# Kernel tuning notes

Hardware: AMD Instinct MI355X
Metric: run time of the kernel (lower is better)

## Reference

```python
import jax, jax.numpy as jnp
import numpy as np

S, B, N, A, L = 2, 8, 12, 4, 24
C, AUX, EK, K, M, OTH = 256, 16, 64, 256, 8, 32
D2 = C + AUX          # transfromer2 d_model
FF = 2048             # torch TransformerEncoderLayer default dim_feedforward
RIN = 2 * EK + 2 * D2 + 2 * OTH
NLAYERS = 2


def _layernorm(x, g, b, eps=1e-5):
    mu = x.mean(-1, keepdims=True)
    var = ((x - mu) ** 2).mean(-1, keepdims=True)
    return (x - mu) * jax.lax.rsqrt(var + eps) * g + b


def _mha(x, Wq, bq, Wk, bk, Wv, bv, Wo, bo):
    # x: [seq, batch, d]; single head (nhead=1), torch seq-first semantics
    q = x @ Wq.T + bq
    k = x @ Wk.T + bk
    v = x @ Wv.T + bv
    scale = x.shape[-1] ** -0.5
    att = jax.nn.softmax(jnp.einsum('sbd,tbd->bst', q, k) * scale, axis=-1)
    o = jnp.einsum('bst,tbd->sbd', att, v)
    return o @ Wo.T + bo


def _encoder(x, aw, ab, w1, b1, w2, b2, lg, lb):
    # post-norm torch TransformerEncoderLayer, ReLU FFN, dropout off (eval)
    for i in range(aw.shape[0]):
        a = _mha(x, aw[i, 0], ab[i, 0], aw[i, 1], ab[i, 1], aw[i, 2], ab[i, 2], aw[i, 3], ab[i, 3])
        x = _layernorm(x + a, lg[i, 0], lb[i, 0])
        h = jax.nn.relu(x @ w1[i].T + b1[i]) @ w2[i].T + b2[i]
        x = _layernorm(x + h, lg[i, 1], lb[i, 1])
    return x


def _conv(x, w, b, pad):
    y = jax.lax.conv_general_dilated(x, w, (1, 1), [(pad, pad), (0, 0)],
                                     dimension_numbers=('NCHW', 'OIHW', 'NCHW'))
    return y + b[None, :, None, None]


def _forward(chars, att_type, kw_idx, input_idx, static, other,
             char_table, filter_w, filter_b, gate_w, gate_b, mlp_w, mlp_b,
             kw_table, aline_w, aline_b,
             t1_attn_w, t1_attn_b, t1_ffn_w1, t1_ffn_b1, t1_ffn_w2, t1_ffn_b2, t1_ln_g, t1_ln_b,
             t2_attn_w, t2_attn_b, t2_ffn_w1, t2_ffn_b1, t2_ffn_w2, t2_ffn_b2, t2_ln_g, t2_ln_b,
             reg_w1, reg_b1, reg_w2, reg_b2):
    # nn.Embedding(max_norm=1): rows renormalized to norm <= 1
    nrm = jnp.linalg.norm(char_table, axis=1, keepdims=True)
    tbl = char_table * jnp.minimum(1.0, 1.0 / jnp.maximum(nrm, 1e-7))
    ce = tbl[chars]                                  # [S,B,N,A,L,C]
    x = ce.reshape(-1, 1, L, C)                      # strings as conv batch
    f = jnp.tanh(_conv(x, filter_w, filter_b, 1))    # gated conv: tanh * sigmoid
    g = jax.nn.sigmoid(_conv(x, gate_w, gate_b, 1))
    v = _conv(f * g, mlp_w, mlp_b, 0)                # 1x1 conv back to 1 channel
    str_vec = v.reshape(S, B, N, A, L, C).mean(axis=4)   # mean over chars -> [S,B,N,A,C]
    kw_vec = kw_table[kw_idx] @ aline_w.T + aline_b      # keyword path -> [S,B,N,A,C]
    att_vec = jnp.where((att_type == 1)[..., None], kw_vec, str_vec)
    # transfromer1: torch seq-first, seq = nodes, batch = (side, plan, attr)
    x1 = att_vec.transpose(2, 0, 1, 3, 4).reshape(N, S * B * A, C)
    y1 = _encoder(x1, t1_attn_w, t1_attn_b, t1_ffn_w1, t1_ffn_b1, t1_ffn_w2, t1_ffn_b2, t1_ln_g, t1_ln_b)
    node_enc = y1.reshape(N, S, B, A, C).mean(axis=3).transpose(1, 2, 0, 3)  # mean over attrs -> [S,B,N,C]
    h = jnp.concatenate([node_enc, static], axis=-1)                          # [S,B,N,D2]
    # transfromer2: seq = plan batch, batch = (side, node) -- torch seq-first
    x2 = h.transpose(1, 0, 2, 3).reshape(B, S * N, D2)
    y2 = _encoder(x2, t2_attn_w, t2_attn_b, t2_ffn_w1, t2_ffn_b1, t2_ffn_w2, t2_ffn_b2, t2_ln_g, t2_ln_b)
    real = y2.reshape(B, S, N, D2).mean(axis=2)      # mean over nodes -> [B,S,D2]
    inp = kw_table[input_idx].mean(axis=2)           # encoding_input -> [S,B,EK]
    feats = jnp.concatenate([inp[0], real[:, 0], inp[1], real[:, 1], other], axis=1)  # [B,RIN]
    return jax.nn.relu(feats @ reg_w1.T + reg_b1) @ reg_w2.T + reg_b2  # [B,1]


def setup_inputs() -> dict:
    key = jax.random.key(0)
    ks = iter(jax.random.split(key, 64))
    def rn(shape, s=0.02):
        return jax.random.normal(next(ks), shape, jnp.float32) * s
    inp = {
        'chars': jax.random.randint(next(ks), (S, B, N, A, L), 0, 128, jnp.int32),
        'att_type': jax.random.randint(next(ks), (S, B, N, A), 0, 2, jnp.int32),
        'kw_idx': jax.random.randint(next(ks), (S, B, N, A), 0, K, jnp.int32),
        'input_idx': jax.random.randint(next(ks), (S, B, M), 0, K, jnp.int32),
        'static': rn((S, B, N, AUX), 1.0),
        'other': rn((B, 2 * OTH), 1.0),
        'char_table': rn((128, C), 1.0),
        'filter_w': rn((16, 1, 3, 1), 0.2), 'filter_b': rn((16,), 0.02),
        'gate_w': rn((16, 1, 3, 1), 0.2), 'gate_b': rn((16,), 0.02),
        'mlp_w': rn((1, 16, 1, 1), 0.2), 'mlp_b': rn((1,), 0.02),
        'kw_table': rn((K, EK), 0.05),
        'aline_w': rn((C, EK), 0.05), 'aline_b': rn((C,), 0.02),
        't1_attn_w': rn((NLAYERS, 4, C, C), 0.05), 't1_attn_b': rn((NLAYERS, 4, C), 0.02),
        't1_ffn_w1': rn((NLAYERS, FF, C), 0.02), 't1_ffn_b1': rn((NLAYERS, FF), 0.02),
        't1_ffn_w2': rn((NLAYERS, C, FF), 0.02), 't1_ffn_b2': rn((NLAYERS, C), 0.02),
        't1_ln_g': jnp.ones((NLAYERS, 2, C), jnp.float32), 't1_ln_b': jnp.zeros((NLAYERS, 2, C), jnp.float32),
        't2_attn_w': rn((NLAYERS, 4, D2, D2), 0.05), 't2_attn_b': rn((NLAYERS, 4, D2), 0.02),
        't2_ffn_w1': rn((NLAYERS, FF, D2), 0.02), 't2_ffn_b1': rn((NLAYERS, FF), 0.02),
        't2_ffn_w2': rn((NLAYERS, D2, FF), 0.02), 't2_ffn_b2': rn((NLAYERS, D2), 0.02),
        't2_ln_g': jnp.ones((NLAYERS, 2, D2), jnp.float32), 't2_ln_b': jnp.zeros((NLAYERS, 2, D2), jnp.float32),
        'reg_w1': rn((32, RIN), 0.05), 'reg_b1': rn((32,), 0.02),
        'reg_w2': rn((1, 32), 0.1), 'reg_b2': rn((1,), 0.02),
    }
    return inp


def reference(chars, att_type, kw_idx, input_idx, static, other,
              char_table, filter_w, filter_b, gate_w, gate_b, mlp_w, mlp_b,
              kw_table, aline_w, aline_b,
              t1_attn_w, t1_attn_b, t1_ffn_w1, t1_ffn_b1, t1_ffn_w2, t1_ffn_b2, t1_ln_g, t1_ln_b,
              t2_attn_w, t2_attn_b, t2_ffn_w1, t2_ffn_b1, t2_ffn_w2, t2_ffn_b2, t2_ln_g, t2_ln_b,
              reg_w1, reg_b1, reg_w2, reg_b2):
    return _forward(chars, att_type, kw_idx, input_idx, static, other,
                    char_table, filter_w, filter_b, gate_w, gate_b, mlp_w, mlp_b,
                    kw_table, aline_w, aline_b,
                    t1_attn_w, t1_attn_b, t1_ffn_w1, t1_ffn_b1, t1_ffn_w2, t1_ffn_b2, t1_ln_g, t1_ln_b,
                    t2_attn_w, t2_attn_b, t2_ffn_w1, t2_ffn_b1, t2_ffn_w2, t2_ffn_b2, t2_ln_g, t2_ln_b,
                    reg_w1, reg_b1, reg_w2, reg_b2)
```

## Files before the change

### kernel.cpp

```cpp
#include <hip/hip_runtime.h>
#include <math.h>

#define S_ 2
#define B_ 8
#define N_ 12
#define A_ 4
#define L_ 24
#define C_ 256
#define AUX_ 16
#define EK_ 64
#define K_ 256
#define M_ 8
#define OTH_ 32
#define D2_ 272
#define FF_ 2048
#define RIN_ 736
#define NSTR_ (S_*B_*N_*A_)
#define NCVT_ 256
#define T4_ (5441536/4)
#define CSZ_ (T4_/NCVT_)

typedef __attribute__((ext_vector_type(8))) short short8v;
typedef __attribute__((ext_vector_type(4))) float f32x4;

// ... 57 lines not shown
        if (tid == 0) su = atomicAdd(ctr, 1);
        __syncthreads();
        int item = su;
        if (item >= NSTR_ + NCVT_) break;

        if (item >= NSTR_) {
            int base = (item - NSTR_) * CSZ_;
            #pragma unroll
            for (int i = 0; i < 6; ++i) {
                int q = base + i * 1024 + tid;
                if (q < base + CSZ_) {
                    int idx = q * 4;
                    const float* src; int off;
                    if      (idx < 524288)  { src = s0; off = 0; }
                    else if (idx < 1572864) { src = s1; off = 524288; }
                    else if (idx < 2621440) { src = s2; off = 1572864; }
                    else if (idx < 3213312) { src = s3; off = 2621440; }
                    else if (idx < 4327424) { src = s4; off = 3213312; }
                    else                    { src = s5; off = 4327424; }
                    float4 v = *(const float4*)(src + (idx - off));
                    ushort4 o;
                    o.x = f2bf(v.x); o.y = f2bf(v.y); o.z = f2bf(v.z); o.w = f2bf(v.w);
                    *(ushort4*)(wdst + idx) = o;
                }
            }
            continue;
        }

        int str = item;
        bool kw = (att_type[str] == 1);
        float partial;
        if (kw) {
            const float* kr = kwt + kw_idx[str] * EK_ + grp * 16;
            const float* awr = aw + c * EK_ + grp * 16;
            float acc = (grp == 0) ? ab[c] : 0.f;
            #pragma unroll
            for (int e = 0; e < 16; ++e) acc = fmaf(kr[e], awr[e], acc);
            partial = acc;
        } else {
            if (tid < L_) ch[tid] = chars[str * L_ + tid];
            __syncthreads();
            #pragma unroll
            for (int i = 0; i < 6; ++i) {
                int l = grp * 6 + i;
                xv[l + 1][c] = tblS[ch[l] * C_ + c];
            }
            if (grp == 0) xv[0][c] = 0.f;
            if (grp == 3) xv[L_ + 1][c] = 0.f;
            __syncthreads();

            float osum[4] = {0.f, 0.f, 0.f, 0.f};
            float xm = xv[0][c], x0 = xv[1][c];
            for (int l = 1; l <= L_; ++l) {
                float xp = xv[l + 1][c];
                #pragma unroll
                for (int oo = 0; oo < 4; ++oo) {
                    float pf2 = fbv[oo] + f0[oo]*xm + f1[oo]*x0 + f2[oo]*xp;
                    float pg  = gbv[oo] + g0[oo]*xm + g1[oo]*x0 + g2[oo]*xp;
                    pf2 = fminf(fmaxf(pf2, -43.f), 43.f);
                    pg  = fminf(fmaxf(pg,  -22.f), 22.f);
                    float e1 = __builtin_amdgcn_exp2f(pf2);
                    float e2 = __builtin_amdgcn_exp2f(pg);
                    float num = (e1 - 1.f) * e2;
                    float den = (e1 + 1.f) * (e2 + 1.f);
                    osum[oo] = fmaf(num, __builtin_amdgcn_rcpf(den), osum[oo]);
                }
                xm = x0; x0 = xp;
            }
            partial = mwv[0]*osum[0] + mwv[1]*osum[1] + mwv[2]*osum[2] + mwv[3]*osum[3];
        }
        part[grp][c] = partial;
        __syncthreads();
        if (grp == 0) {
            int a = str & 3;
            int n = (str >> 2) % N_;
            int sb = str / (N_ * A_);
            int row = n * 64 + sb * 4 + a;
            float tot = part[0][c] + part[1][c] + part[2][c] + part[3][c];
            float out = kw ? tot : (mb[0] + tot * (1.f / 24.f));
            x1[row * C_ + c] = out;
            x1b[row * C_ + c] = f2bf(out);
        }
    }
}

__global__ void gemm_mfma_k(const unsigned short* __restrict__ Ab,
                            const unsigned short* __restrict__ Wb,
                            const float* __restrict__ bias,
                            float* __restrict__ Cf, unsigned short* __restrict__ Cb,
                            int R, int K, int N, int relu, int kslice, int obf) {
    int tid = threadIdx.x;
    int wave = tid >> 6, lane = tid & 63;
    int fr = lane & 15, fq = lane >> 4;
    int m0 = blockIdx.y * 64;
    int n0 = blockIdx.x * 64 + wave * 16;
    int kbeg = blockIdx.z * kslice;
    int kend = min(kbeg + kslice, K);
    int col = n0 + fr;
    bool bok = col < N;
    const unsigned short* Wrow = Wb + (size_t)col * K;
    const unsigned short* Ar0 = Ab + (size_t)(m0 + fr) * K;
    const unsigned short* Ar1 = Ab + (size_t)(m0 + 16 + fr) * K;
    const unsigned short* Ar2 = Ab + (size_t)(m0 + 32 + fr) * K;
    const unsigned short* Ar3 = Ab + (size_t)(m0 + 48 + fr) * K;

    f32x4 acc0 = {0.f,0.f,0.f,0.f}, acc1 = {0.f,0.f,0.f,0.f};
    f32x4 acc2 = {0.f,0.f,0.f,0.f}, acc3 = {0.f,0.f,0.f,0.f};
    const short8v z8 = {0,0,0,0,0,0,0,0};
    short8v pb0, pa00, pa01, pa02, pa03;
    short8v pb1, pa10, pa11, pa12, pa13;

#define LDSET(PB,PA0,PA1,PA2,PA3,ktv) do {                                \
        int kl2 = (ktv) + fq * 8;                                         \
        bool kv2 = (kl2 + 8 <= kend);                                     \
        PB  = (bok && kv2) ? *(const short8v*)(Wrow + kl2) : z8;          \
        PA0 = kv2 ? *(const short8v*)(Ar0 + kl2) : z8;                    \
        PA1 = kv2 ? *(const short8v*)(Ar1 + kl2) : z8;                    \
        PA2 = kv2 ? *(const short8v*)(Ar2 + kl2) : z8;                    \
        PA3 = kv2 ? *(const short8v*)(Ar3 + kl2) : z8;                    \
    } while (0)

    if (kbeg < kend) {
        LDSET(pb0, pa00, pa01, pa02, pa03, kbeg);
        LDSET(pb1, pa10, pa11, pa12, pa13, kbeg + 32);
        for (int kt = kbeg; kt < kend; kt += 64) {
            short8v tb = pb0, t0 = pa00, t1 = pa01, t2 = pa02, t3 = pa03;
            LDSET(pb0, pa00, pa01, pa02, pa03, kt + 64);
            acc0 = __builtin_amdgcn_mfma_f32_16x16x32_bf16(t0, tb, acc0, 0, 0, 0);
            acc1 = __builtin_amdgcn_mfma_f32_16x16x32_bf16(t1, tb, acc1, 0, 0, 0);
            acc2 = __builtin_amdgcn_mfma_f32_16x16x32_bf16(t2, tb, acc2, 0, 0, 0);
            acc3 = __builtin_amdgcn_mfma_f32_16x16x32_bf16(t3, tb, acc3, 0, 0, 0);
            short8v ub = pb1, u0 = pa10, u1 = pa11, u2 = pa12, u3 = pa13;
            LDSET(pb1, pa10, pa11, pa12, pa13, kt + 96);
            acc0 = __builtin_amdgcn_mfma_f32_16x16x32_bf16(u0, ub, acc0, 0, 0, 0);
            acc1 = __builtin_amdgcn_mfma_f32_16x16x32_bf16(u1, ub, acc1, 0, 0, 0);
            acc2 = __builtin_amdgcn_mfma_f32_16x16x32_bf16(u2, ub, acc2, 0, 0, 0);
            acc3 = __builtin_amdgcn_mfma_f32_16x16x32_bf16(u3, ub, acc3, 0, 0, 0);
        }
    }
#undef LDSET

    if (!bok) return;
    bool direct = (gridDim.z == 1);
    float bv = direct ? bias[col] : 0.f;
    float* outf = direct ? Cf : (Cf + (size_t)blockIdx.z * R * N);
#define STOREACC(accv, mi) do {                                           \
        _Pragma("unroll")                                                 \
        for (int j = 0; j < 4; ++j) {                                     \
            int row = m0 + (mi)*16 + fq * 4 + j;                          \
            float v = accv[j] + bv;                                       \
            if (direct && relu) v = fmaxf(v, 0.f);                        \
            if (direct && obf) Cb[(size_t)row * N + col] = f2bf(v);       \
            else               outf[(size_t)row * N + col] = v;           \
        }                                                                 \
    } while (0)
    STOREACC(acc0, 0); STOREACC(acc1, 1); STOREACC(acc2, 2); STOREACC(acc3, 3);
#undef STOREACC
}

__global__ void redln_k(const float* __restrict__ part, const float* __restrict__ bias,
                        float* __restrict__ x, unsigned short* __restrict__ xb,
                        const float* __restrict__ g, const float* __restrict__ b,
                        int d, int NS, int RN) {
    int r = blockIdx.x, tid = threadIdx.x;
    __shared__ float red[10];
    const float* xr = x + (size_t)r * d;
    int i0 = tid, i1 = tid + 256;
    bool h0 = i0 < d, h1 = i1 < d;
    float v0 = 0.f, v1 = 0.f;
    if (h0) {
        v0 = xr[i0] + bias[i0];
        for (int z = 0; z < NS; ++z) v0 += part[(size_t)z * RN + (size_t)r * d + i0];
    }
    if (h1) {
        v1 = xr[i1] + bias[i1];
        for (int z = 0; z < NS; ++z) v1 += part[(size_t)z * RN + (size_t)r * d + i1];
    }
    float s = v0 + v1, ss = v0 * v0 + v1 * v1;
    for (int off = 32; off; off >>= 1) {
        s += __shfl_down(s, off);
        ss += __shfl_down(ss, off);
    }
    if ((tid & 63) == 0) { red[(tid >> 6) * 2] = s; red[(tid >> 6) * 2 + 1] = ss; }
    __syncthreads();
    if (tid == 0) {
        float S = red[0] + red[2] + red[4] + red[6];
        float SS = red[1] + red[3] + red[5] + red[7];
        float mu = S / d;
        float var = SS / d - mu * mu;
        red[8] = mu;
        red[9] = rsqrtf(var + 1e-5f);
    }
    __syncthreads();
    float mu = red[8], inv = red[9];
    float* xw = x + (size_t)r * d;
    if (h0) {
        float o = (v0 - mu) * inv * g[i0] + b[i0];
        xw[i0] = o; xb[(size_t)r * d + i0] = f2bf(o);
    }
    if (h1) {
        float o = (v1 - mu) * inv * g[i1] + b[i1];
        xw[i1] = o; xb[(size_t)r * d + i1] = f2bf(o);
    }
}

__global__ void attn_k(const float* __restrict__ qkv, unsigned short* __restrict__ ob,
                       int seq, int batch, int d, float scale) {
    __shared__ float sm[3 * 12 * 260];
    __shared__ float sc[12 * 12];
    int j = blockIdx.x, tid = threadIdx.x;
    int dp = d + 4;
    int s3 = 3 * d;
    float* qs = sm;
    float* ks = sm + 12 * 260;
    float* vs = sm + 2 * 12 * 260;
    for (int idx = tid; idx < seq * d; idx += 256) {
        int s = idx / d, cc = idx - s * d;
        const float* base = qkv + (size_t)(s * batch + j) * s3 + cc;
        qs[s * dp + cc] = base[0];
        ks[s * dp + cc] = base[d];
        vs[s * dp + cc] = base[2 * d];
    }
    __syncthreads();
    for (int p4 = tid; p4 < seq * seq * 4; p4 += 256) {
        int p = p4 >> 2, sub = p4 & 3;
        int s = p / seq, t = p - s * seq;
        const float* qp = qs + s * dp;
        const float* kp = ks + t * dp;
        float acc = 0.f;
        for (int cc = sub; cc < d; cc += 4) acc = fmaf(qp[cc], kp[cc], acc);
        acc += __shfl_xor(acc, 1);
        acc += __shfl_xor(acc, 2);
        if (sub == 0) sc[p] = acc * scale;
    }
    __syncthreads();
    if (tid < seq) {
        float m = -1e30f;
        for (int t = 0; t < seq; ++t) m = fmaxf(m, sc[tid * seq + t]);
        float ssum = 0.f;
        for (int t = 0; t < seq; ++t) {
            float e = __expf(sc[tid * seq + t] - m);
            sc[tid * seq + t] = e;
            ssum += e;
        }
        float inv = 1.f / ssum;
        for (int t = 0; t < seq; ++t) sc[tid * seq + t] *= inv;
    }
    __syncthreads();
    for (int c = tid; c < d; c += 256) {
        for (int s = 0; s < seq; ++s) {
            float acc = 0.f;
            for (int t = 0; t < seq; ++t) acc = fmaf(sc[s * seq + t], vs[t * dp + c], acc);
            ob[(size_t)(s * batch + j) * d + c] = f2bf(acc);
        }
    }
}

__global__ void build_x2_k(const float* __restrict__ y1, const float* __restrict__ stat,
                           float* __restrict__ x2, unsigned short* __restrict__ x2b) {
    int id = blockIdx.x;
    int n = id % N_;
    int b = (id / N_) % B_;
    int s = id / (N_ * B_);
    int orow = b * (S_ * N_) + s * N_ + n;
    for (int c = threadIdx.x; c < D2_; c += 256) {
        float v;
        if (c < C_) {
            int j0 = (s * B_ + b) * A_;
            float acc = 0.f;
            for (int a = 0; a < A_; ++a) acc += y1[(size_t)(n * 64 + j0 + a) * C_ + c];
            v = acc * 0.25f;
        } else {
            v = stat[((size_t)(s * B_ + b) * N_ + n) * AUX_ + (c - C_)];
        }
        x2[(size_t)orow * D2_ + c] = v;
        x2b[(size_t)orow * D2_ + c] = f2bf(v);
    }
}

__global__ void regressor_k(const float* __restrict__ y2, const int* __restrict__ input_idx,
                            const float* __restrict__ kwt, const float* __restrict__ other,
                            const float* __restrict__ w1, const float* __restrict__ b1,
                            const float* __restrict__ w2, const float* __restrict__ b2,
                            float* __restrict__ out) {
    int b = blockIdx.x;
    int tid = threadIdx.x;
    __shared__ float realsh[2][D2_];
    __shared__ float feats[RIN_];
    __shared__ float hh[32];
    for (int idx = tid; idx < 2 * D2_; idx += 256) {
        int s = idx / D2_, c = idx - s * D2_;
        float acc = 0.f;
        for (int n = 0; n < N_; ++n)
            acc += y2[(size_t)(b * 24 + s * N_ + n) * D2_ + c];
        realsh[s][c] = acc * (1.f / 12.f);
    }
    __syncthreads();
    for (int i = tid; i < RIN_; i += 256) {
        float v;
        if (i < 64) {
            float acc = 0.f;
            for (int m = 0; m < M_; ++m) acc += kwt[input_idx[b * M_ + m] * EK_ + i];
            v = acc * 0.125f;
        } else if (i < 336) {
            v = realsh[0][i - 64];
        } else if (i < 400) {
            int e = i - 336;
            float acc = 0.f;
            for (int m = 0; m < M_; ++m) acc += kwt[input_idx[64 + b * M_ + m] * EK_ + e];
            v = acc * 0.125f;
        } else if (i < 672) {
            v = realsh[1][i - 400];
        } else {
            v = other[b * 64 + (i - 672)];
        }
        feats[i] = v;
    }
    __syncthreads();
    if (tid < 32) {
        float acc = b1[tid];
        const float* wr = w1 + (size_t)tid * RIN_;
        for (int i = 0; i < RIN_; ++i) acc += feats[i] * wr[i];
        hh[tid] = fmaxf(acc, 0.f);
    }
    __syncthreads();
    if (tid == 0) {
        float acc = b2[0];
        for (int j = 0; j < 32; ++j) acc += hh[j] * w2[j];
        out[b] = acc;
    }
}

extern "C" void kernel_launch(void* const* d_in, const int* in_sizes, int n_in,
                              void* d_out, int out_size, void* d_ws, size_t ws_size,
                              hipStream_t stream) {
    const int*   chars      = (const int*)d_in[0];
    const int*   att_type   = (const int*)d_in[1];
    const int*   kw_idx     = (const int*)d_in[2];
    const int*   input_idx  = (const int*)d_in[3];
    const float* stat       = (const float*)d_in[4];
    const float* other      = (const float*)d_in[5];
    const float* char_table = (const float*)d_in[6];
    const float* filter_w   = (const float*)d_in[7];
    const float* filter_b   = (const float*)d_in[8];
    const float* gate_w     = (const float*)d_in[9];
    const float* gate_b     = (const float*)d_in[10];
    const float* mlp_w      = (const float*)d_in[11];
    const float* mlp_b      = (const float*)d_in[12];
    const float* kw_table   = (const float*)d_in[13];
    const float* aline_w    = (const float*)d_in[14];
    const float* aline_b    = (const float*)d_in[15];
    const float* t1_attn_w  = (const float*)d_in[16];
    const float* t1_attn_b  = (const float*)d_in[17];
    const float* t1_ffn_w1  = (const float*)d_in[18];
    const float* t1_ffn_b1  = (const float*)d_in[19];
    const float* t1_ffn_w2  = (const float*)d_in[20];
    const float* t1_ffn_b2  = (const float*)d_in[21];
    const float* t1_ln_g    = (const float*)d_in[22];
    const float* t1_ln_b    = (const float*)d_in[23];
    const float* t2_attn_w  = (const float*)d_in[24];
    const float* t2_attn_b  = (const float*)d_in[25];
    const float* t2_ffn_w1  = (const float*)d_in[26];
    const float* t2_ffn_b1  = (const float*)d_in[27];
    const float* t2_ffn_w2  = (const float*)d_in[28];
    const float* t2_ffn_b2  = (const float*)d_in[29];
    const float* t2_ln_g    = (const float*)d_in[30];
    const float* t2_ln_b    = (const float*)d_in[31];
    const float* reg_w1     = (const float*)d_in[32];
    const float* reg_b1     = (const float*)d_in[33];
    const float* reg_w2     = (const float*)d_in[34];
    const float* reg_b2     = (const float*)d_in[35];

    float* ws   = (float*)d_ws;
    float* tblS = ws;
    float* x1   = tblS + 32768;
    float* qkv  = x1 + 196608;
    float* pbuf = qkv + 589824;
    float* x2   = pbuf + 786432;
    float* spare= x2 + 52224;
    unsigned short* x1b = (unsigned short*)(spare + 4352);
    unsigned short* obb = x1b + 196608;
    unsigned short* hb  = obb + 196608;
    unsigned short* x2b = hb + 1572864;
    unsigned short* wbf = x2b + 52224 + 16;
    unsigned short* wb_t1_attn = wbf;
    unsigned short* wb_t1_ffn1 = wbf + 524288;
    unsigned short* wb_t1_ffn2 = wbf + 1572864;
    unsigned short* wb_t2_attn = wbf + 2621440;
    unsigned short* wb_t2_ffn1 = wbf + 3213312;
    unsigned short* wb_t2_ffn2 = wbf + 4327424;
    int* ctr = (int*)(wbf + 5441536);

    auto gemm_f32 = [&](const unsigned short* A, const unsigned short* Wb, const float* bias,
                        float* Cc, int R, int Kk, int N) {
        dim3 g((N + 63) / 64, R / 64, 1);
        gemm_mfma_k<<<g, 256, 0, stream>>>(A, Wb, bias, Cc, (unsigned short*)0,
                                           R, Kk, N, 0, Kk, 0);
    };
    auto gemm_bf16 = [&](const unsigned short* A, const unsigned short* Wb, const float* bias,
                         unsigned short* Cc, int R, int Kk, int N) {
        dim3 g((N + 63) / 64, R / 64, 1);
        gemm_mfma_k<<<g, 256, 0, stream>>>(A, Wb, bias, (float*)0, Cc,
                                           R, Kk, N, 1, Kk, 1);
    };
    auto gemm_split_ln = [&](const unsigned short* A, const unsigned short* Wb,
                             const float* bias, float* x, unsigned short* xb,
                             const float* g, const float* b,
                             int R, int Kk, int N, int ns) {
        int ksl = ((Kk + ns - 1) / ns + 31) / 32 * 32;
        dim3 gr((N + 63) / 64, R / 64, ns);
        gemm_mfma_k<<<gr, 256, 0, stream>>>(A, Wb, bias, pbuf, (unsigned short*)0,
                                            R, Kk, N, 0, ksl, 0);
        redln_k<<<R, 256, 0, stream>>>(pbuf, bias, x, xb, g, b, N, ns, R * N);
    };

    hipMemsetAsync(ctr, 0, sizeof(int), stream);
    scale_table_k<<<128, 256, 0, stream>>>(char_table, tblS);
    attvec_k<<<512, 1024, 0, stream>>>(chars, att_type, kw_idx, tblS,
                                       filter_w, filter_b, gate_w, gate_b,
                                       mlp_w, mlp_b, kw_table, aline_w, aline_b,
                                       x1, x1b, ctr,
                                       t1_attn_w, t1_ffn_w1, t1_ffn_w2,
                                       t2_attn_w, t2_ffn_w1, t2_ffn_w2, wbf);

    for (int i = 0; i < 2; ++i) {
        const unsigned short* awb = wb_t1_attn + (size_t)i * 4 * C_ * C_;
        const float* ab = t1_attn_b + (size_t)i * 4 * C_;
        gemm_f32(x1b, awb, ab, qkv, 768, C_, 3 * C_);
        attn_k<<<64, 256, 0, stream>>>(qkv, obb, 12, 64, C_, 0.0625f);
        gemm_split_ln(obb, awb + 3 * C_ * C_, ab + 3 * C_, x1, x1b,
                      t1_ln_g + i * 2 * C_, t1_ln_b + i * 2 * C_, 768, C_, C_, 2);
        gemm_bf16(x1b, wb_t1_ffn1 + (size_t)i * FF_ * C_, t1_ffn_b1 + i * FF_, hb, 768, C_, FF_);
        gemm_split_ln(hb, wb_t1_ffn2 + (size_t)i * C_ * FF_, t1_ffn_b2 + i * C_, x1, x1b,
                      t1_ln_g + i * 2 * C_ + C_, t1_ln_b + i * 2 * C_ + C_, 768, FF_, C_, 4);
    }

    build_x2_k<<<192, 256, 0, stream>>>(x1, stat, x2, x2b);

    float sc2 = 1.0f / sqrtf(272.0f);
    for (int i = 0; i < 2; ++i) {
        const unsigned short* awb = wb_t2_attn + (size_t)i * 4 * D2_ * D2_;
        const float* ab = t2_attn_b + (size_t)i * 4 * D2_;
        gemm_f32(x2b, awb, ab, qkv, 192, D2_, 3 * D2_);
        attn_k<<<24, 256, 0, stream>>>(qkv, obb, 8, 24, D2_, sc2);
        gemm_split_ln(obb, awb + 3 * D2_ * D2_, ab + 3 * D2_, x2, x2b,
                      t2_ln_g + i * 2 * D2_, t2_ln_b + i * 2 * D2_, 192, D2_, D2_, 4);
        gemm_bf16(x2b, wb_t2_ffn1 + (size_t)i * FF_ * D2_, t2_ffn_b1 + i * FF_, hb, 192, D2_, FF_);
        gemm_split_ln(hb, wb_t2_ffn2 + (size_t)i * D2_ * FF_, t2_ffn_b2 + i * D2_, x2, x2b,
                      t2_ln_g + i * 2 * D2_ + D2_, t2_ln_b + i * 2 * D2_ + D2_, 192, FF_, D2_, 8);
    }

    regressor_k<<<8, 256, 0, stream>>>(x2, input_idx, kw_table, other,
                                       reg_w1, reg_b1, reg_w2, reg_b2, (float*)d_out);
}
```

Baseline: 321.8 us.

## Fuse QKV projection, attention, output projection and residual LayerNorm into one kernel

Replaces the four-launch attention sublayer (QKV GEMM, attention kernel, split-K output GEMM, and reduction plus LayerNorm) with one templated kernel per batch column. Each block computes its sequence's QKV with MFMA into shared memory, runs softmax attention, applies the output projection with MFMA, and does the residual add and LayerNorm in place. The aim is to cut launch overhead and the global round-trips of the qkv, attention output and partial-sum buffers. In exchange, each block reloads the full attention weights from L2, and only 64 or 24 blocks do the projection work, so GPU parallelism is lower.

```diff
diff --git a/kernel.cpp b/kernel.cpp
--- a/kernel.cpp
+++ b/kernel.cpp
@@ -285,54 +285,159 @@
     }
 }
 
-__global__ void attn_k(const float* __restrict__ qkv, unsigned short* __restrict__ ob,
-                       int seq, int batch, int d, float scale) {
-    __shared__ float sm[3 * 12 * 260];
-    __shared__ float sc[12 * 12];
-    int j = blockIdx.x, tid = threadIdx.x;
-    int dp = d + 4;
-    int s3 = 3 * d;
-    float* qs = sm;
-    float* ks = sm + 12 * 260;
-    float* vs = sm + 2 * 12 * 260;
-    for (int idx = tid; idx < seq * d; idx += 256) {
-        int s = idx / d, cc = idx - s * d;
-        const float* base = qkv + (size_t)(s * batch + j) * s3 + cc;
-        qs[s * dp + cc] = base[0];
-        ks[s * dp + cc] = base[d];
-        vs[s * dp + cc] = base[2 * d];
-    }
-    __syncthreads();
-    for (int p4 = tid; p4 < seq * seq * 4; p4 += 256) {
+template<int SEQ, int BATCH, int D>
+__global__ void attn_fused_k(const unsigned short* __restrict__ xb,
+                             float* __restrict__ x,
+                             const unsigned short* __restrict__ wqkv,
+                             const float* __restrict__ bqkv,
+                             const unsigned short* __restrict__ wo,
+                             const float* __restrict__ bo,
+                             const float* __restrict__ lng,
+                             const float* __restrict__ lnb,
+                             unsigned short* __restrict__ xb_out,
+                             float scale) {
+    constexpr int N3 = 3 * D;
+    constexpr int NF1 = (N3 / 16 + 3) / 4;
+    constexpr int NF2 = (D / 16 + 3) / 4;
+    constexpr int QP = N3 + 8;
+    constexpr int OP = D + 8;
+    constexpr int NSTEP = (D + 31) / 32;
+    constexpr int NCH = (D + 63) / 64;
+
+    __shared__ float qkv[16][QP];
+    __shared__ unsigned short ob[16][OP];
+    __shared__ float outp[16][OP];
+    __shared__ float sc[16 * 16];
+
+    int j = blockIdx.x;
+    int tid = threadIdx.x;
+    int wave = tid >> 6, lane = tid & 63;
+    int fr = lane & 15, fq = lane >> 4;
+    const short8v z8 = {0,0,0,0,0,0,0,0};
+
+    const unsigned short* Arow = xb + ((size_t)fr * BATCH + j) * D;
+    bool arok = fr < SEQ;
+    f32x4 acc[NF1];
+    #pragma unroll
+    for (int u = 0; u < NF1; ++u) acc[u] = (f32x4){0.f,0.f,0.f,0.f};
+    #pragma unroll
+    for (int st = 0; st < NSTEP; ++st) {
+        int kl = st * 32 + fq * 8;
+        bool kv = (kl + 8 <= D);
+        short8v af = (arok && kv) ? *(const short8v*)(Arow + kl) : z8;
+        #pragma unroll
+        for (int u = 0; u < NF1; ++u) {
+            int fi = wave + 4 * u;
+            if (fi * 16 < N3) {
+                short8v bf = kv ? *(const short8v*)(wqkv + (size_t)(fi * 16 + fr) * D + kl) : z8;
+                acc[u] = __builtin_amdgcn_mfma_f32_16x16x32_bf16(af, bf, acc[u], 0, 0, 0);
+            }
+        }
+    }
+    #pragma unroll
+    for (int u = 0; u < NF1; ++u) {
+        int fi = wave + 4 * u;
+        if (fi * 16 < N3) {
+            int col = fi * 16 + fr;
+            float bv = bqkv[col];
+            #pragma unroll
+            for (int jj = 0; jj < 4; ++jj)
+                qkv[fq * 4 + jj][col] = acc[u][jj] + bv;
+        }
+    }
+    __syncthreads();
+
+    for (int p4 = tid; p4 < SEQ * SEQ * 4; p4 += 256) {
         int p = p4 >> 2, sub = p4 & 3;
-        int s = p / seq, t = p - s * seq;
-        const float* qp = qs + s * dp;
-        const float* kp = ks + t * dp;
-        float acc = 0.f;
-        for (int cc = sub; cc < d; cc += 4) acc = fmaf(qp[cc], kp[cc], acc);
-        acc += __shfl_xor(acc, 1);
-        acc += __shfl_xor(acc, 2);
-        if (sub == 0) sc[p] = acc * scale;
-    }
-    __syncthreads();
-    if (tid < seq) {
+        int s = p / SEQ, t = p - s * SEQ;
+        float a = 0.f;
+        for (int cc = sub; cc < D; cc += 4)
+            a = fmaf(qkv[s][cc], qkv[t][D + cc], a);
+        a += __shfl_xor(a, 1);
+        a += __shfl_xor(a, 2);
+        if (sub == 0) sc[s * SEQ + t] = a * scale;
+    }
+    __syncthreads();
+    if (tid < SEQ) {
         float m = -1e30f;
-        for (int t = 0; t < seq; ++t) m = fmaxf(m, sc[tid * seq + t]);
+        for (int t = 0; t < SEQ; ++t) m = fmaxf(m, sc[tid * SEQ + t]);
         float ssum = 0.f;
-        for (int t = 0; t < seq; ++t) {
-            float e = __expf(sc[tid * seq + t] - m);
-            sc[tid * seq + t] = e;
-            ssum += e;
+        for (int t = 0; t < SEQ; ++t) {
+            float e = __expf(sc[tid * SEQ + t] - m);
+            sc[tid * SEQ + t] = e; ssum += e;
         }
         float inv = 1.f / ssum;
-        for (int t = 0; t < seq; ++t) sc[tid * seq + t] *= inv;
-    }
-    __syncthreads();
-    for (int c = tid; c < d; c += 256) {
-        for (int s = 0; s < seq; ++s) {
-            float acc = 0.f;
-            for (int t = 0; t < seq; ++t) acc = fmaf(sc[s * seq + t], vs[t * dp + c], acc);
-            ob[(size_t)(s * batch + j) * d + c] = f2bf(acc);
+        for (int t = 0; t < SEQ; ++t) sc[tid * SEQ + t] *= inv;
+    }
+    __syncthreads();
+    for (int c = tid; c < D; c += 256) {
+        #pragma unroll
+        for (int s = 0; s < 16; ++s) {
+            float a = 0.f;
+            if (s < SEQ)
+                for (int t = 0; t < SEQ; ++t)
+                    a = fmaf(sc[s * SEQ + t], qkv[t][2 * D + c], a);
+            ob[s][c] = f2bf(a);
+        }
+    }
+    __syncthreads();
+
+    f32x4 acc2[NF2];
+    #pragma unroll
+    for (int u = 0; u < NF2; ++u) acc2[u] = (f32x4){0.f,0.f,0.f,0.f};
+    #pragma unroll
+    for (int st = 0; st < NSTEP; ++st) {
+        int kl = st * 32 + fq * 8;
+        bool kv = (kl + 8 <= D);
+        short8v af = kv ? *(const short8v*)(&ob[fr][kl]) : z8;
+        #pragma unroll
+        for (int u = 0; u < NF2; ++u) {
+            int fi = wave + 4 * u;
+            if (fi * 16 < D) {
+                short8v bf = kv ? *(const short8v*)(wo + (size_t)(fi * 16 + fr) * D + kl) : z8;
+                acc2[u] = __builtin_amdgcn_mfma_f32_16x16x32_bf16(af, bf, acc2[u], 0, 0, 0);
+            }
+        }
+    }
+    #pragma unroll
+    for (int u = 0; u < NF2; ++u) {
+        int fi = wave + 4 * u;
+        if (fi * 16 < D) {
+            int col = fi * 16 + fr;
+            float bv = bo[col];
+            #pragma unroll
+            for (int jj = 0; jj < 4; ++jj)
+                outp[fq * 4 + jj][col] = acc2[u][jj] + bv;
+        }
+    }
+    __syncthreads();
+
+    for (int r = wave; r < SEQ; r += 4) {
+        size_t g = (size_t)r * BATCH + j;
+        float v[NCH];
+        float s = 0.f, ss = 0.f;
+        #pragma unroll
+        for (int q = 0; q < NCH; ++q) {
+            int cc = lane + q * 64;
+            float val = 0.f;
+            if (cc < D) val = outp[r][cc] + x[g * D + cc];
+            v[q] = val; s += val; ss += val * val;
+        }
+        #pragma unroll
+        for (int off = 32; off; off >>= 1) {
+            s += __shfl_xor(s, off);
+            ss += __shfl_xor(ss, off);
+        }
+        float mu = s / D;
+        float inv = rsqrtf(ss / D - mu * mu + 1e-5f);
+        #pragma unroll
+        for (int q = 0; q < NCH; ++q) {
+            int cc = lane + q * 64;
+            if (cc < D) {
+                float o = (v[q] - mu) * inv * lng[cc] + lnb[cc];
+                x[g * D + cc] = o;
+                xb_out[g * D + cc] = f2bf(o);
+            }
         }
     }
 }
@@ -472,12 +577,6 @@
     unsigned short* wb_t2_ffn2 = wbf + 4327424;
     int* ctr = (int*)(wbf + 5441536);
 
-    auto gemm_f32 = [&](const unsigned short* A, const unsigned short* Wb, const float* bias,
-                        float* Cc, int R, int Kk, int N) {
-        dim3 g((N + 63) / 64, R / 64, 1);
-        gemm_mfma_k<<<g, 256, 0, stream>>>(A, Wb, bias, Cc, (unsigned short*)0,
-                                           R, Kk, N, 0, Kk, 0);
-    };
     auto gemm_bf16 = [&](const unsigned short* A, const unsigned short* Wb, const float* bias,
                          unsigned short* Cc, int R, int Kk, int N) {
         dim3 g((N + 63) / 64, R / 64, 1);
@@ -507,10 +606,9 @@
     for (int i = 0; i < 2; ++i) {
         const unsigned short* awb = wb_t1_attn + (size_t)i * 4 * C_ * C_;
         const float* ab = t1_attn_b + (size_t)i * 4 * C_;
-        gemm_f32(x1b, awb, ab, qkv, 768, C_, 3 * C_);
-        attn_k<<<64, 256, 0, stream>>>(qkv, obb, 12, 64, C_, 0.0625f);
-        gemm_split_ln(obb, awb + 3 * C_ * C_, ab + 3 * C_, x1, x1b,
-                      t1_ln_g + i * 2 * C_, t1_ln_b + i * 2 * C_, 768, C_, C_, 2);
+        attn_fused_k<12, 64, 256><<<64, 256, 0, stream>>>(
+            x1b, x1, awb, ab, awb + 3 * C_ * C_, ab + 3 * C_,
+            t1_ln_g + i * 2 * C_, t1_ln_b + i * 2 * C_, x1b, 0.0625f);
         gemm_bf16(x1b, wb_t1_ffn1 + (size_t)i * FF_ * C_, t1_ffn_b1 + i * FF_, hb, 768, C_, FF_);
         gemm_split_ln(hb, wb_t1_ffn2 + (size_t)i * C_ * FF_, t1_ffn_b2 + i * C_, x1, x1b,
                       t1_ln_g + i * 2 * C_ + C_, t1_ln_b + i * 2 * C_ + C_, 768, FF_, C_, 4);
@@ -522,10 +620,9 @@
     for (int i = 0; i < 2; ++i) {
         const unsigned short* awb = wb_t2_attn + (size_t)i * 4 * D2_ * D2_;
         const float* ab = t2_attn_b + (size_t)i * 4 * D2_;
-        gemm_f32(x2b, awb, ab, qkv, 192, D2_, 3 * D2_);
-        attn_k<<<24, 256, 0, stream>>>(qkv, obb, 8, 24, D2_, sc2);
-        gemm_split_ln(obb, awb + 3 * D2_ * D2_, ab + 3 * D2_, x2, x2b,
-                      t2_ln_g + i * 2 * D2_, t2_ln_b + i * 2 * D2_, 192, D2_, D2_, 4);
+        attn_fused_k<8, 24, 272><<<24, 256, 0, stream>>>(
+            x2b, x2, awb, ab, awb + 3 * D2_ * D2_, ab + 3 * D2_,
+            t2_ln_g + i * 2 * D2_, t2_ln_b + i * 2 * D2_, x2b, sc2);
         gemm_bf16(x2b, wb_t2_ffn1 + (size_t)i * FF_ * D2_, t2_ffn_b1 + i * FF_, hb, 192, D2_, FF_);
         gemm_split_ln(hb, wb_t2_ffn2 + (size_t)i * D2_ * FF_, t2_ffn_b2 + i * D2_, x2, x2b,
                       t2_ln_g + i * 2 * D2_ + D2_, t2_ln_b + i * 2 * D2_ + D2_, 192, FF_, D2_, 8);
```

After: 344.9 us. 7.2% more time.

## Fuse FFN up-projection, ReLU and down-projection into one kernel per hidden slice

Applied to the files above, without the earlier changes.

Replaces the separate FFN1 GEMM (bf16 hidden written to global) and split-K FFN2 GEMM with a single kernel in which each block computes a 64-row by 256-hidden slice, keeps the ReLU output in LDS, and multiplies it by the matching W2 slice into per-slice partial sums. The existing reduce+layernorm kernel then sums the 8 partials. This removes the global round trip of the 768x2048 hidden activation and one launch per layer. The cost is far fewer blocks (96 and 24), weights read straight from global without LDS staging, and more partial-sum traffic than before.

```diff
diff --git a/kernel.cpp b/kernel.cpp
--- a/kernel.cpp
+++ b/kernel.cpp
@@ -237,6 +237,107 @@
     } while (0)
     STOREACC(acc0, 0); STOREACC(acc1, 1); STOREACC(acc2, 2); STOREACC(acc3, 3);
 #undef STOREACC
+}
+
+template<int D, int NF2>
+__global__ void ffn_fused_k(const unsigned short* __restrict__ xb,
+                            const unsigned short* __restrict__ w1,
+                            const float* __restrict__ b1,
+                            const unsigned short* __restrict__ w2,
+                            float* __restrict__ pbuf, int R) {
+    constexpr int HS = 256;
+    constexpr int NSTEP1 = (D + 31) / 32;
+    int tid = threadIdx.x;
+    int wave = tid >> 6, lane = tid & 63;
+    int fr = lane & 15, fq = lane >> 4;
+    int m0 = blockIdx.x * 64;
+    int z  = blockIdx.y;
+    int h0 = z * HS;
+    __shared__ unsigned short hsm[64][HS + 8];
+    const short8v z8 = {0,0,0,0,0,0,0,0};
+
+    const unsigned short* Ar0 = xb + (size_t)(m0 + fr) * D;
+    const unsigned short* Ar1 = xb + (size_t)(m0 + 16 + fr) * D;
+    const unsigned short* Ar2 = xb + (size_t)(m0 + 32 + fr) * D;
+    const unsigned short* Ar3 = xb + (size_t)(m0 + 48 + fr) * D;
+
+    f32x4 a1[4][4];
+    #pragma unroll
+    for (int mi = 0; mi < 4; ++mi)
+        #pragma unroll
+        for (int f = 0; f < 4; ++f) a1[mi][f] = (f32x4){0.f,0.f,0.f,0.f};
+    #pragma unroll
+    for (int st = 0; st < NSTEP1; ++st) {
+        int kl = st * 32 + fq * 8;
+        bool kv = (kl + 8 <= D);
+        short8v af0 = kv ? *(const short8v*)(Ar0 + kl) : z8;
+        short8v af1 = kv ? *(const short8v*)(Ar1 + kl) : z8;
+        short8v af2 = kv ? *(const short8v*)(Ar2 + kl) : z8;
+        short8v af3 = kv ? *(const short8v*)(Ar3 + kl) : z8;
+        #pragma unroll
+        for (int f = 0; f < 4; ++f) {
+            int hh = h0 + wave * 64 + f * 16 + fr;
+            short8v bf = kv ? *(const short8v*)(w1 + (size_t)hh * D + kl) : z8;
+            a1[0][f] = __builtin_amdgcn_mfma_f32_16x16x32_bf16(af0, bf, a1[0][f], 0, 0, 0);
+            a1[1][f] = __builtin_amdgcn_mfma_f32_16x16x32_bf16(af1, bf, a1[1][f], 0, 0, 0);
+            a1[2][f] = __builtin_amdgcn_mfma_f32_16x16x32_bf16(af2, bf, a1[2][f], 0, 0, 0);
+            a1[3][f] = __builtin_amdgcn_mfma_f32_16x16x32_bf16(af3, bf, a1[3][f], 0, 0, 0);
+        }
+    }
+    #pragma unroll
+    for (int f = 0; f < 4; ++f) {
+        int coll = wave * 64 + f * 16 + fr;
+        float bv = b1[h0 + coll];
+        #pragma unroll
+        for (int mi = 0; mi < 4; ++mi)
+            #pragma unroll
+            for (int jj = 0; jj < 4; ++jj) {
+                float v = fmaxf(a1[mi][f][jj] + bv, 0.f);
+                hsm[mi * 16 + fq * 4 + jj][coll] = f2bf(v);
+            }
+    }
+    __syncthreads();
+
+    f32x4 a2[4][NF2];
+    #pragma unroll
+    for (int mi = 0; mi < 4; ++mi)
+        #pragma unroll
+        for (int u = 0; u < NF2; ++u) a2[mi][u] = (f32x4){0.f,0.f,0.f,0.f};
+    #pragma unroll
+    for (int st = 0; st < HS / 32; ++st) {
+        int kl = st * 32 + fq * 8;
+        short8v af0 = *(const short8v*)(&hsm[fr][kl]);
+        short8v af1 = *(const short8v*)(&hsm[16 + fr][kl]);
+        short8v af2 = *(const short8v*)(&hsm[32 + fr][kl]);
+        short8v af3 = *(const short8v*)(&hsm[48 + fr][kl]);
+        #pragma unroll
+        for (int u = 0; u < NF2; ++u) {
+            int fi = wave + 4 * u;
+            if (fi * 16 < D) {
+                int n = fi * 16 + fr;
+                short8v bf = *(const short8v*)(w2 + (size_t)n * FF_ + h0 + kl);
+                a2[0][u] = __builtin_amdgcn_mfma_f32_16x16x32_bf16(af0, bf, a2[0][u], 0, 0, 0);
+                a2[1][u] = __builtin_amdgcn_mfma_f32_16x16x32_bf16(af1, bf, a2[1][u], 0, 0, 0);
+                a2[2][u] = __builtin_amdgcn_mfma_f32_16x16x32_bf16(af2, bf, a2[2][u], 0, 0, 0);
+                a2[3][u] = __builtin_amdgcn_mfma_f32_16x16x32_bf16(af3, bf, a2[3][u], 0, 0, 0);
+            }
+        }
+    }
+    float* pp = pbuf + (size_t)z * R * D;
+    #pragma unroll
+    for (int u = 0; u < NF2; ++u) {
+        int fi = wave + 4 * u;
+        if (fi * 16 < D) {
+            int n = fi * 16 + fr;
+            #pragma unroll
+            for (int mi = 0; mi < 4; ++mi)
+                #pragma unroll
+                for (int jj = 0; jj < 4; ++jj) {
+                    int row = m0 + mi * 16 + fq * 4 + jj;
+                    pp[(size_t)row * D + n] = a2[mi][u][jj];
+                }
+        }
+    }
 }
 
 __global__ void redln_k(const float* __restrict__ part, const float* __restrict__ bias,
@@ -457,12 +558,10 @@
     float* x1   = tblS + 32768;
     float* qkv  = x1 + 196608;
     float* pbuf = qkv + 589824;
-    float* x2   = pbuf + 786432;
-    float* spare= x2 + 52224;
-    unsigned short* x1b = (unsigned short*)(spare + 4352);
+    float* x2   = pbuf + 1572864;
+    unsigned short* x1b = (unsigned short*)(x2 + 52224);
     unsigned short* obb = x1b + 196608;
-    unsigned short* hb  = obb + 196608;
-    unsigned short* x2b = hb + 1572864;
+    unsigned short* x2b = obb + 196608;
     unsigned short* wbf = x2b + 52224 + 16;
     unsigned short* wb_t1_attn = wbf;
     unsigned short* wb_t1_ffn1 = wbf + 524288;
@@ -477,12 +576,6 @@
         dim3 g((N + 63) / 64, R / 64, 1);
         gemm_mfma_k<<<g, 256, 0, stream>>>(A, Wb, bias, Cc, (unsigned short*)0,
                                            R, Kk, N, 0, Kk, 0);
-    };
-    auto gemm_bf16 = [&](const unsigned short* A, const unsigned short* Wb, const float* bias,
-                         unsigned short* Cc, int R, int Kk, int N) {
-        dim3 g((N + 63) / 64, R / 64, 1);
-        gemm_mfma_k<<<g, 256, 0, stream>>>(A, Wb, bias, (float*)0, Cc,
-                                           R, Kk, N, 1, Kk, 1);
     };
     auto gemm_split_ln = [&](const unsigned short* A, const unsigned short* Wb,
                              const float* bias, float* x, unsigned short* xb,
@@ -511,9 +604,12 @@
         attn_k<<<64, 256, 0, stream>>>(qkv, obb, 12, 64, C_, 0.0625f);
         gemm_split_ln(obb, awb + 3 * C_ * C_, ab + 3 * C_, x1, x1b,
                       t1_ln_g + i * 2 * C_, t1_ln_b + i * 2 * C_, 768, C_, C_, 2);
-        gemm_bf16(x1b, wb_t1_ffn1 + (size_t)i * FF_ * C_, t1_ffn_b1 + i * FF_, hb, 768, C_, FF_);
-        gemm_split_ln(hb, wb_t1_ffn2 + (size_t)i * C_ * FF_, t1_ffn_b2 + i * C_, x1, x1b,
-                      t1_ln_g + i * 2 * C_ + C_, t1_ln_b + i * 2 * C_ + C_, 768, FF_, C_, 4);
+        ffn_fused_k<256, 4><<<dim3(12, 8), 256, 0, stream>>>(
+            x1b, wb_t1_ffn1 + (size_t)i * FF_ * C_, t1_ffn_b1 + i * FF_,
+            wb_t1_ffn2 + (size_t)i * C_ * FF_, pbuf, 768);
+        redln_k<<<768, 256, 0, stream>>>(pbuf, t1_ffn_b2 + i * C_, x1, x1b,
+                                         t1_ln_g + i * 2 * C_ + C_, t1_ln_b + i * 2 * C_ + C_,
+                                         C_, 8, 768 * C_);
     }
 
     build_x2_k<<<192, 256, 0, stream>>>(x1, stat, x2, x2b);
@@ -526,9 +622,12 @@
         attn_k<<<24, 256, 0, stream>>>(qkv, obb, 8, 24, D2_, sc2);
         gemm_split_ln(obb, awb + 3 * D2_ * D2_, ab + 3 * D2_, x2, x2b,
                       t2_ln_g + i * 2 * D2_, t2_ln_b + i * 2 * D2_, 192, D2_, D2_, 4);
-        gemm_bf16(x2b, wb_t2_ffn1 + (size_t)i * FF_ * D2_, t2_ffn_b1 + i * FF_, hb, 192, D2_, FF_);
-        gemm_split_ln(hb, wb_t2_ffn2 + (size_t)i * D2_ * FF_, t2_ffn_b2 + i * D2_, x2, x2b,
-                      t2_ln_g + i * 2 * D2_ + D2_, t2_ln_b + i * 2 * D2_ + D2_, 192, FF_, D2_, 8);
+        ffn_fused_k<272, 5><<<dim3(3, 8), 256, 0, stream>>>(
+            x2b, wb_t2_ffn1 + (size_t)i * FF_ * D2_, t2_ffn_b1 + i * FF_,
+            wb_t2_ffn2 + (size_t)i * D2_ * FF_, pbuf, 192);
+        redln_k<<<192, 256, 0, stream>>>(pbuf, t2_ffn_b2 + i * D2_, x2, x2b,
+                                         t2_ln_g + i * 2 * D2_ + D2_, t2_ln_b + i * 2 * D2_ + D2_,
+                                         D2_, 8, 192 * D2_);
     }
 
     regressor_k<<<8, 256, 0, stream>>>(x2, input_idx, kw_table, other,
```

After: 338.6 us. +5.2%, slower.

## Fuse split-K reduction and LayerNorm into the next GEMM's prologue

Applied to the files above, without the earlier changes.

Adds a gemm_pro kernel that sums the split-K partials, adds the residual and bias, applies LayerNorm into an LDS bf16 tile, and then runs the following GEMM (FFN1 or next layer's QKV) from that tile. This removes most standalone redln launches and the bf16 activation round-trip through global memory. Residual buffers are now ping-ponged because the LN output is written by the first column block. The cost is that every column block recomputes the reduction and LayerNorm for its 64 rows and reads the full partial buffer, and the B operand is loaded directly from global memory without LDS staging.

```diff
diff --git a/kernel.cpp b/kernel.cpp
--- a/kernel.cpp
+++ b/kernel.cpp
@@ -233,6 +233,93 @@
             if (direct && relu) v = fmaxf(v, 0.f);                        \
             if (direct && obf) Cb[(size_t)row * N + col] = f2bf(v);       \
             else               outf[(size_t)row * N + col] = v;           \
+        }                                                                 \
+    } while (0)
+    STOREACC(acc0, 0); STOREACC(acc1, 1); STOREACC(acc2, 2); STOREACC(acc3, 3);
+#undef STOREACC
+}
+
+__global__ void gemm_pro_k(const float* __restrict__ part, int NS,
+                           const float* __restrict__ xres,
+                           const float* __restrict__ bias_p,
+                           const float* __restrict__ lng, const float* __restrict__ lnb,
+                           float* __restrict__ x_out,
+                           const unsigned short* __restrict__ Wb,
+                           const float* __restrict__ bias,
+                           float* __restrict__ Cf, unsigned short* __restrict__ Cb,
+                           int R, int K, int N, int relu, int obf) {
+    __shared__ unsigned short lnA[64][280];
+    int tid = threadIdx.x;
+    int wave = tid >> 6, lane = tid & 63;
+    int fr = lane & 15, fq = lane >> 4;
+    int m0 = blockIdx.y * 64;
+    int n0 = blockIdx.x * 64 + wave * 16;
+    const short8v z8 = {0,0,0,0,0,0,0,0};
+
+    for (int i = 0; i < 16; ++i) {
+        int r = m0 + wave * 16 + i;
+        size_t g = (size_t)r * K;
+        float v[5];
+        float s = 0.f, ss = 0.f;
+        #pragma unroll
+        for (int q = 0; q < 5; ++q) {
+            int cc = lane + q * 64;
+            float val = 0.f;
+            if (cc < K) {
+                val = xres[g + cc] + bias_p[cc];
+                for (int z = 0; z < NS; ++z)
+                    val += part[(size_t)z * R * K + g + cc];
+            }
+            v[q] = val; s += val; ss += val * val;
+        }
+        #pragma unroll
+        for (int off = 32; off; off >>= 1) {
+            s += __shfl_xor(s, off);
+            ss += __shfl_xor(ss, off);
+        }
+        float mu = s / K;
+        float inv = rsqrtf(ss / K - mu * mu + 1e-5f);
+        #pragma unroll
+        for (int q = 0; q < 5; ++q) {
+            int cc = lane + q * 64;
+            if (cc < K) {
+                float o = (v[q] - mu) * inv * lng[cc] + lnb[cc];
+                lnA[wave * 16 + i][cc] = f2bf(o);
+                if (blockIdx.x == 0) x_out[g + cc] = o;
+            }
+        }
+    }
+    __syncthreads();
+
+    int col = n0 + fr;
+    bool bok = col < N;
+    const unsigned short* Wrow = Wb + (size_t)col * K;
+    f32x4 acc0 = {0.f,0.f,0.f,0.f}, acc1 = {0.f,0.f,0.f,0.f};
+    f32x4 acc2 = {0.f,0.f,0.f,0.f}, acc3 = {0.f,0.f,0.f,0.f};
+    for (int kt = 0; kt < K; kt += 32) {
+        int kl = kt + fq * 8;
+        bool kv = (kl + 8 <= K);
+        short8v bf  = (bok && kv) ? *(const short8v*)(Wrow + kl) : z8;
+        short8v af0 = kv ? *(const short8v*)(&lnA[fr][kl])      : z8;
+        short8v af1 = kv ? *(const short8v*)(&lnA[16 + fr][kl]) : z8;
+        short8v af2 = kv ? *(const short8v*)(&lnA[32 + fr][kl]) : z8;
+        short8v af3 = kv ? *(const short8v*)(&lnA[48 + fr][kl]) : z8;
+        acc0 = __builtin_amdgcn_mfma_f32_16x16x32_bf16(af0, bf, acc0, 0, 0, 0);
+        acc1 = __builtin_amdgcn_mfma_f32_16x16x32_bf16(af1, bf, acc1, 0, 0, 0);
+        acc2 = __builtin_amdgcn_mfma_f32_16x16x32_bf16(af2, bf, acc2, 0, 0, 0);
+        acc3 = __builtin_amdgcn_mfma_f32_16x16x32_bf16(af3, bf, acc3, 0, 0, 0);
+    }
+
+    if (!bok) return;
+    float bv = bias[col];
+#define STOREACC(accv, mi) do {                                           \
+        _Pragma("unroll")                                                 \
+        for (int j = 0; j < 4; ++j) {                                     \
+            int row = m0 + (mi)*16 + fq * 4 + j;                          \
+            float v = accv[j] + bv;                                       \
+            if (relu) v = fmaxf(v, 0.f);                                  \
+            if (obf) Cb[(size_t)row * N + col] = f2bf(v);                 \
+            else     Cf[(size_t)row * N + col] = v;                       \
         }                                                                 \
     } while (0)
     STOREACC(acc0, 0); STOREACC(acc1, 1); STOREACC(acc2, 2); STOREACC(acc3, 3);
@@ -454,13 +541,14 @@
 
     float* ws   = (float*)d_ws;
     float* tblS = ws;
-    float* x1   = tblS + 32768;
-    float* qkv  = x1 + 196608;
+    float* xA   = tblS + 32768;
+    float* xB   = xA + 196608;
+    float* qkv  = xB + 196608;
     float* pbuf = qkv + 589824;
-    float* x2   = pbuf + 786432;
-    float* spare= x2 + 52224;
-    unsigned short* x1b = (unsigned short*)(spare + 4352);
-    unsigned short* obb = x1b + 196608;
+    float* x2A  = pbuf + 786432;
+    float* x2B  = x2A + 52224;
+    unsigned short* xb0 = (unsigned short*)(x2B + 52224);
+    unsigned short* obb = xb0 + 196608;
     unsigned short* hb  = obb + 196608;
     unsigned short* x2b = hb + 1572864;
     unsigned short* wbf = x2b + 52224 + 16;
@@ -478,21 +566,21 @@
         gemm_mfma_k<<<g, 256, 0, stream>>>(A, Wb, bias, Cc, (unsigned short*)0,
                                            R, Kk, N, 0, Kk, 0);
     };
-    auto gemm_bf16 = [&](const unsigned short* A, const unsigned short* Wb, const float* bias,
-                         unsigned short* Cc, int R, int Kk, int N) {
-        dim3 g((N + 63) / 64, R / 64, 1);
-        gemm_mfma_k<<<g, 256, 0, stream>>>(A, Wb, bias, (float*)0, Cc,
-                                           R, Kk, N, 1, Kk, 1);
-    };
-    auto gemm_split_ln = [&](const unsigned short* A, const unsigned short* Wb,
-                             const float* bias, float* x, unsigned short* xb,
-                             const float* g, const float* b,
-                             int R, int Kk, int N, int ns) {
+    auto gemm_part = [&](const unsigned short* A, const unsigned short* Wb,
+                         int R, int Kk, int N, int ns) {
         int ksl = ((Kk + ns - 1) / ns + 31) / 32 * 32;
         dim3 gr((N + 63) / 64, R / 64, ns);
-        gemm_mfma_k<<<gr, 256, 0, stream>>>(A, Wb, bias, pbuf, (unsigned short*)0,
-                                            R, Kk, N, 0, ksl, 0);
-        redln_k<<<R, 256, 0, stream>>>(pbuf, bias, x, xb, g, b, N, ns, R * N);
+        gemm_mfma_k<<<gr, 256, 0, stream>>>(A, Wb, (const float*)0, pbuf,
+                                            (unsigned short*)0, R, Kk, N, 0, ksl, 0);
+    };
+    auto gemm_pro = [&](int ns, const float* xres, const float* bias_p,
+                        const float* lng, const float* lnb, float* x_out,
+                        const unsigned short* Wb, const float* bias,
+                        float* Cf, unsigned short* Cb,
+                        int R, int Kk, int N, int relu, int obf) {
+        dim3 g((N + 63) / 64, R / 64, 1);
+        gemm_pro_k<<<g, 256, 0, stream>>>(pbuf, ns, xres, bias_p, lng, lnb, x_out,
+                                          Wb, bias, Cf, Cb, R, Kk, N, relu, obf);
     };
 
     hipMemsetAsync(ctr, 0, sizeof(int), stream);
@@ -500,37 +588,61 @@
     attvec_k<<<512, 1024, 0, stream>>>(chars, att_type, kw_idx, tblS,
                                        filter_w, filter_b, gate_w, gate_b,
                                        mlp_w, mlp_b, kw_table, aline_w, aline_b,
-                                       x1, x1b, ctr,
+                                       xA, xb0, ctr,
                                        t1_attn_w, t1_ffn_w1, t1_ffn_w2,
                                        t2_attn_w, t2_ffn_w1, t2_ffn_w2, wbf);
 
-    for (int i = 0; i < 2; ++i) {
-        const unsigned short* awb = wb_t1_attn + (size_t)i * 4 * C_ * C_;
-        const float* ab = t1_attn_b + (size_t)i * 4 * C_;
-        gemm_f32(x1b, awb, ab, qkv, 768, C_, 3 * C_);
+    {
+        const unsigned short* awb0 = wb_t1_attn;
+        const unsigned short* awb1 = wb_t1_attn + (size_t)4 * C_ * C_;
+        const float* ab0 = t1_attn_b;
+        const float* ab1 = t1_attn_b + 4 * C_;
+        gemm_f32(xb0, awb0, ab0, qkv, 768, C_, 3 * C_);
         attn_k<<<64, 256, 0, stream>>>(qkv, obb, 12, 64, C_, 0.0625f);
-        gemm_split_ln(obb, awb + 3 * C_ * C_, ab + 3 * C_, x1, x1b,
-                      t1_ln_g + i * 2 * C_, t1_ln_b + i * 2 * C_, 768, C_, C_, 2);
-        gemm_bf16(x1b, wb_t1_ffn1 + (size_t)i * FF_ * C_, t1_ffn_b1 + i * FF_, hb, 768, C_, FF_);
-        gemm_split_ln(hb, wb_t1_ffn2 + (size_t)i * C_ * FF_, t1_ffn_b2 + i * C_, x1, x1b,
-                      t1_ln_g + i * 2 * C_ + C_, t1_ln_b + i * 2 * C_ + C_, 768, FF_, C_, 4);
-    }
-
-    build_x2_k<<<192, 256, 0, stream>>>(x1, stat, x2, x2b);
+        gemm_part(obb, awb0 + 3 * C_ * C_, 768, C_, C_, 2);
+        gemm_pro(2, xA, ab0 + 3 * C_, t1_ln_g, t1_ln_b, xB,
+                 wb_t1_ffn1, t1_ffn_b1, (float*)0, hb, 768, C_, FF_, 1, 1);
+        gemm_part(hb, wb_t1_ffn2, 768, FF_, C_, 4);
+        gemm_pro(4, xB, t1_ffn_b2, t1_ln_g + C_, t1_ln_b + C_, xA,
+                 awb1, ab1, qkv, (unsigned short*)0, 768, C_, 3 * C_, 0, 0);
+        attn_k<<<64, 256, 0, stream>>>(qkv, obb, 12, 64, C_, 0.0625f);
+        gemm_part(obb, awb1 + 3 * C_ * C_, 768, C_, C_, 2);
+        gemm_pro(2, xA, ab1 + 3 * C_, t1_ln_g + 2 * C_, t1_ln_b + 2 * C_, xB,
+                 wb_t1_ffn1 + (size_t)FF_ * C_, t1_ffn_b1 + FF_, (float*)0, hb,
+                 768, C_, FF_, 1, 1);
+        gemm_part(hb, wb_t1_ffn2 + (size_t)C_ * FF_, 768, FF_, C_, 4);
+        redln_k<<<768, 256, 0, stream>>>(pbuf, t1_ffn_b2 + C_, xB, xb0,
+                                         t1_ln_g + 3 * C_, t1_ln_b + 3 * C_,
+                                         C_, 4, 768 * C_);
+    }
+
+    build_x2_k<<<192, 256, 0, stream>>>(xB, stat, x2A, x2b);
 
     float sc2 = 1.0f / sqrtf(272.0f);
-    for (int i = 0; i < 2; ++i) {
-        const unsigned short* awb = wb_t2_attn + (size_t)i * 4 * D2_ * D2_;
-        const float* ab = t2_attn_b + (size_t)i * 4 * D2_;
-        gemm_f32(x2b, awb, ab, qkv, 192, D2_, 3 * D2_);
+    {
+        const unsigned short* awb0 = wb_t2_attn;
+        const unsigned short* awb1 = wb_t2_attn + (size_t)4 * D2_ * D2_;
+        const float* ab0 = t2_attn_b;
+        const float* ab1 = t2_attn_b + 4 * D2_;
+        gemm_f32(x2b, awb0, ab0, qkv, 192, D2_, 3 * D2_);
         attn_k<<<24, 256, 0, stream>>>(qkv, obb, 8, 24, D2_, sc2);
-        gemm_split_ln(obb, awb + 3 * D2_ * D2_, ab + 3 * D2_, x2, x2b,
-                      t2_ln_g + i * 2 * D2_, t2_ln_b + i * 2 * D2_, 192, D2_, D2_, 4);
-        gemm_bf16(x2b, wb_t2_ffn1 + (size_t)i * FF_ * D2_, t2_ffn_b1 + i * FF_, hb, 192, D2_, FF_);
-        gemm_split_ln(hb, wb_t2_ffn2 + (size_t)i * D2_ * FF_, t2_ffn_b2 + i * D2_, x2, x2b,
-                      t2_ln_g + i * 2 * D2_ + D2_, t2_ln_b + i * 2 * D2_ + D2_, 192, FF_, D2_, 8);
-    }
-
-    regressor_k<<<8, 256, 0, stream>>>(x2, input_idx, kw_table, other,
+        gemm_part(obb, awb0 + 3 * D2_ * D2_, 192, D2_, D2_, 4);
+        gemm_pro(4, x2A, ab0 + 3 * D2_, t2_ln_g, t2_ln_b, x2B,
+                 wb_t2_ffn1, t2_ffn_b1, (float*)0, hb, 192, D2_, FF_, 1, 1);
+        gemm_part(hb, wb_t2_ffn2, 192, FF_, D2_, 8);
+        gemm_pro(8, x2B, t2_ffn_b2, t2_ln_g + D2_, t2_ln_b + D2_, x2A,
+                 awb1, ab1, qkv, (unsigned short*)0, 192, D2_, 3 * D2_, 0, 0);
+        attn_k<<<24, 256, 0, stream>>>(qkv, obb, 8, 24, D2_, sc2);
+        gemm_part(obb, awb1 + 3 * D2_ * D2_, 192, D2_, D2_, 4);
+        gemm_pro(4, x2A, ab1 + 3 * D2_, t2_ln_g + 2 * D2_, t2_ln_b + 2 * D2_, x2B,
+                 wb_t2_ffn1 + (size_t)FF_ * D2_, t2_ffn_b1 + FF_, (float*)0, hb,
+                 192, D2_, FF_, 1, 1);
+        gemm_part(hb, wb_t2_ffn2 + (size_t)D2_ * FF_, 192, FF_, D2_, 8);
+        redln_k<<<192, 256, 0, stream>>>(pbuf, t2_ffn_b2 + D2_, x2B, x2b,
+                                         t2_ln_g + 3 * D2_, t2_ln_b + 3 * D2_,
+                                         D2_, 8, 192 * D2_);
+    }
+
+    regressor_k<<<8, 256, 0, stream>>>(x2B, input_idx, kw_table, other,
                                        reg_w1, reg_b1, reg_w2, reg_b2, (float*)d_out);
 }
```

Measured after the change: 888.6 us. 176% more time.
